# Kernel tuning notes

Measured on AMD Instinct MI355X. Metric: run time of the kernel, lower is better.

## Reference

```python
import jax, jax.numpy as jnp
import numpy as np

IMG = 840.0
MIN_SIZES = [[16.0, 32.0], [64.0, 128.0], [256.0, 512.0]]
STEPS = [8, 16, 32]
THRESH = 0.35      # neg_overlap / matching threshold used by this repo's MultiBoxLoss
NEG_POS = 7
LOC_WEIGHT = 2.0
VAR0, VAR1 = 0.1, 0.2


def _make_priors():
    out = []
    for ms, step in zip(MIN_SIZES, STEPS):
        f = int(np.ceil(IMG / step))
        jj, ii = np.meshgrid(np.arange(f), np.arange(f))  # j: cols (x), i: rows (y)
        cx = (jj + 0.5) * step / IMG
        cy = (ii + 0.5) * step / IMG
        for m in ms:
            s = np.full_like(cx, m / IMG)
            out.append(np.stack([cx, cy, s, s], axis=-1).reshape(-1, 4))
    return np.concatenate(out, axis=0).astype(np.float32)  # [29126, 4] (cx, cy, w, h)


def setup_inputs() -> dict:
    key = jax.random.key(0)
    k1, k2, k3, k4 = jax.random.split(key, 4)
    B, G = 64, 24
    priors = jnp.asarray(_make_priors())            # [P, 4]
    P = priors.shape[0]
    loc_data = 0.1 * jax.random.normal(k1, (B, P, 4), dtype=jnp.float32)
    conf_data = jax.random.normal(k2, (B, P, 2), dtype=jnp.float32)
    cxy = jax.random.uniform(k3, (B, G, 2), minval=0.2, maxval=0.8)
    wh = jax.random.uniform(k4, (B, G, 2), minval=0.05, maxval=0.3)
    gt_boxes = jnp.clip(jnp.concatenate([cxy - wh / 2, cxy + wh / 2], axis=-1), 1e-3, 1.0)
    gt_labels = jnp.ones((B, G), dtype=jnp.int32)   # single foreground class (num_classes=2)
    return {"loc_data": loc_data, "conf_data": conf_data, "gt_boxes": gt_boxes,
            "gt_labels": gt_labels, "priors": priors}


def _multibox_loss(loc_data, conf_data, gt_boxes, gt_labels, priors):
    B, P, _ = loc_data.shape
    G = gt_boxes.shape[1]
    # priors in point form for IoU
    pr_pt = jnp.concatenate([priors[:, :2] - priors[:, 2:] / 2,
                             priors[:, :2] + priors[:, 2:] / 2], axis=1)  # [P,4]
    area_p = (pr_pt[:, 2] - pr_pt[:, 0]) * (pr_pt[:, 3] - pr_pt[:, 1])

    def match_one(truths, labels):
        # IoU [G, P]
        lt = jnp.maximum(truths[:, None, :2], pr_pt[None, :, :2])
        rb = jnp.minimum(truths[:, None, 2:], pr_pt[None, :, 2:])
        wh = jnp.clip(rb - lt, 0.0)
        inter = wh[..., 0] * wh[..., 1]
        area_t = (truths[:, 2] - truths[:, 0]) * (truths[:, 3] - truths[:, 1])
        iou = inter / (area_t[:, None] + area_p[None, :] - inter)
        best_prior_idx = jnp.argmax(iou, axis=1)          # [G]
        bto = jnp.max(iou, axis=0)                        # [P] best truth overlap
        bti = jnp.argmax(iou, axis=0)                     # [P] best truth idx
        bto = bto.at[best_prior_idx].set(2.0)             # ensure each gt keeps its best prior
        bti = bti.at[best_prior_idx].set(jnp.arange(G))
        matched = truths[bti]                             # [P,4]
        conf = jnp.where(bto < THRESH, 0, labels[bti])    # [P]
        # encode (SSD style, variances 0.1/0.2)
        g_cxcy = ((matched[:, :2] + matched[:, 2:]) / 2 - priors[:, :2]) / (VAR0 * priors[:, 2:])
        g_wh = jnp.log((matched[:, 2:] - matched[:, :2]) / priors[:, 2:]) / VAR1
        return jnp.concatenate([g_cxcy, g_wh], axis=1), conf

    loc_t, conf_t = jax.vmap(match_one)(gt_boxes, gt_labels)  # [B,P,4], [B,P]
    pos = conf_t > 0                                          # [B,P]

    # localization: smooth L1 over positives
    diff = jnp.abs(loc_data - loc_t)
    sl1 = jnp.where(diff < 1.0, 0.5 * diff * diff, diff - 0.5)
    loss_l = jnp.sum(sl1 * pos[..., None].astype(loc_data.dtype))

    # per-prior CE = logsumexp - logit[target]
    lse = jax.nn.logsumexp(conf_data, axis=-1)                               # [B,P]
    gold = jnp.take_along_axis(conf_data, conf_t[..., None], axis=-1)[..., 0]
    ce_all = lse - gold                                                      # [B,P]

    # hard negative mining: rank background-class loss of negatives
    mine = jnp.where(pos, 0.0, ce_all)
    rank = jnp.argsort(jnp.argsort(-mine, axis=1), axis=1)
    num_pos = jnp.sum(pos, axis=1, keepdims=True)                            # [B,1]
    num_neg = jnp.minimum(NEG_POS * num_pos, P - 1)
    neg = rank < num_neg

    mask = pos | neg
    loss_c = jnp.sum(jnp.where(mask, ce_all, 0.0))

    N = jnp.maximum(jnp.sum(pos).astype(loc_data.dtype), 1.0)
    return loss_l / N, loss_c / N


def reference(loc_data, conf_data, gt_boxes, gt_labels, priors):
    loss_l, loss_c = _multibox_loss(loc_data, conf_data, gt_boxes, gt_labels, priors)
    return LOC_WEIGHT * loss_l + loss_c
```

## Files before the change

### kernel.cpp

```cpp
#include <hip/hip_runtime.h>

static constexpr int B_ = 64;
static constexpr int P_ = 29126;
static constexpr int G_ = 24;
static constexpr float THRESH_ = 0.35f;
static constexpr int NEGPOS_ = 7;
static constexpr int PBC_ = (P_ + 2047) / 2048;
static constexpr int NBLK_ = PBC_ * B_;
static constexpr int CCSTRIDE_ = 32;

static constexpr size_t ZBYTES_ =
    (size_t)B_*P_ + (size_t)B_*4096*4 + (size_t)B_*CCSTRIDE_*4;
static constexpr int ZVEC_ = (int)((ZBYTES_ + 15) / 16);

__global__ __launch_bounds__(256) void k_zero(ulonglong2* __restrict__ dst)
{
    const int i = blockIdx.x*256 + threadIdx.x;
    if (i < ZVEC_) dst[i] = make_ulonglong2(0ull, 0ull);
}

__global__ __launch_bounds__(256) void k_sparse(
    const float4* __restrict__ gt4,
    const float4* __restrict__ priors4,
    unsigned char* __restrict__ match,
    unsigned long long* __restrict__ bp_pack)
{
    const int g = blockIdx.x;
    const int b = blockIdx.y;
    const int bg = b*G_ + g;
    const int tid = threadIdx.x;

    const float4 t = gt4[bg];
    const float area_t = (t.z - t.x) * (t.w - t.y);

    float bv = -1.0f; int bq = 0;

#pragma unroll
    for (int r = 0; r < 6; ++r) {
        const int   f    = (r < 2) ? 105 : (r < 4) ? 53 : 27;
        const float sc   = (r < 2) ? 105.0f : (r < 4) ? 52.5f : 26.25f;
        const int   base = (r == 0) ? 0 : (r == 1) ? 11025 : (r == 2) ? 22050
                         : (r == 3) ? 24859 : (r == 4) ? 27668 : 28397;
        const float hw   = ((r == 0) ? 16.0f : (r == 1) ? 32.0f : (r == 2) ? 64.0f
                         : (r == 3) ? 128.0f : (r == 4) ? 256.0f : 512.0f)
                           * (0.5f / 840.0f);

        const int j0 = max(0,     (int)floorf((t.x - hw)*sc - 0.5f) - 1);
        const int j1 = min(f - 1, (int)ceilf ((t.z + hw)*sc - 0.5f) + 1);
        const int i0 = max(0,     (int)floorf((t.y - hw)*sc - 0.5f) - 1);
        const int i1 = min(f - 1, (int)ceilf ((t.w + hw)*sc - 0.5f) + 1);
        const int W = j1 - j0 + 1;
        const int n = W * (i1 - i0 + 1);

        for (int c = tid; c < n; c += 256) {
            const int ii = c / W;
            const int jj = c - ii*W;
            const int p = base + (i0 + ii)*f + (j0 + jj);
            const float4 pr = priors4[p];
            const float hx = pr.z * 0.5f, hy = pr.w * 0.5f;
            const float px0 = pr.x - hx, py0 = pr.y - hy;
            const float px1 = pr.x + hx, py1 = pr.y + hy;
            const float area_p = (px1 - px0) * (py1 - py0);
            const float lx = fmaxf(t.x, px0), ly = fmaxf(t.y, py0);
            const float rx = fminf(t.z, px1), ry = fminf(t.w, py1);
            const float iw = fmaxf(rx - lx, 0.0f), ih = fmaxf(ry - ly, 0.0f);
            const float inter = iw * ih;
            const float iou = __fdividef(inter, (area_t + area_p) - inter);

            if (iou >= THRESH_) match[(size_t)b*P_ + p] = 1;
            if (iou > bv) { bv = iou; bq = p; }
        }
    }

    const int lane = tid & 63, wave = tid >> 6;
    for (int m = 32; m; m >>= 1) {
        const float ov = __shfl_xor(bv, m, 64);
        const int   oq = __shfl_xor(bq, m, 64);
        if (ov > bv || (ov == bv && oq < bq)) { bv = ov; bq = oq; }
    }
    __shared__ float swv[4];
    __shared__ int   swq[4];
    if (lane == 0) { swv[wave] = bv; swq[wave] = bq; }
    __syncthreads();
    if (tid == 0) {
        float v = swv[0]; int q = swq[0];
#pragma unroll
        for (int w = 1; w < 4; ++w)
            if (swv[w] > v || (swv[w] == v && swq[w] < q)) { v = swv[w]; q = swq[w]; }
        bp_pack[bg] = (v >= 0.0f)
            ? (((unsigned long long)__float_as_uint(v) << 32)
               | (unsigned long long)(~(unsigned int)q))
            : 0ull;
    }
}

__global__ __launch_bounds__(256) void k_loss(
    const float4* __restrict__ loc4,
    const float2* __restrict__ conf2,
    const float4* __restrict__ gt4,
    const int* __restrict__ labels,
    const float4* __restrict__ priors4,
    const unsigned char* __restrict__ match,
    const unsigned long long* __restrict__ bp_pack,
    float* __restrict__ mine,
    float* __restrict__ pl, float* __restrict__ pc, int* __restrict__ pp,
    unsigned int* __restrict__ hist1)
{
    const int b = blockIdx.y;
    const int tid = threadIdx.x;
    __shared__ float4 sgt[G_];
    __shared__ float  sarea[G_];
    __shared__ int    sbpi[G_];
    __shared__ int    slab[G_];
    __shared__ unsigned int shist[4096];
    if (tid < G_) {
        const float4 t = gt4[b*G_ + tid];
        sgt[tid] = t;
        sarea[tid] = (t.z - t.x) * (t.w - t.y);
        sbpi[tid] = (int)(~(unsigned int)(bp_pack[b*G_ + tid] & 0xFFFFFFFFull));
        slab[tid] = labels[b*G_ + tid];
    }
    for (int i = tid; i < 4096; i += 256) shist[i] = 0;
    __syncthreads();

    float lL = 0.0f, pce = 0.0f; int np = 0;

#pragma unroll
    for (int c = 0; c < 8; ++c) {
        const int p = blockIdx.x*2048 + c*256 + tid;
        if (p < P_) {
            const int idx = b*P_ + p;
            const unsigned char fl = match[idx];

            int og = -1;
#pragma unroll
            for (int g = 0; g < G_; ++g)
                if (sbpi[g] == p) og = g;

            int cc = 0, g = 0;
            if (og >= 0) { g = og; cc = slab[g]; }
            else if (fl) {
                const float4 pr = priors4[p];
                const float hx = pr.z * 0.5f, hy = pr.w * 0.5f;
                const float px0 = pr.x - hx, py0 = pr.y - hy;
                const float px1 = pr.x + hx, py1 = pr.y + hy;
                const float area_p = (px1 - px0) * (py1 - py0);
                float best = -1.0f;
#pragma unroll
                for (int gg = 0; gg < G_; ++gg) {
                    const float4 t = sgt[gg];
                    const float lx = fmaxf(t.x, px0), ly = fmaxf(t.y, py0);
                    const float rx = fminf(t.z, px1), ry = fminf(t.w, py1);
                    const float iw = fmaxf(rx - lx, 0.0f), ih = fmaxf(ry - ly, 0.0f);
                    const float inter = iw * ih;
                    const float iou = __fdividef(inter, (sarea[gg] + area_p) - inter);
                    if (iou > best) { best = iou; g = gg; }
                }
                cc = slab[g];
            }

            const float2 x = conf2[idx];
            const float z = (cc == 0) ? (x.y - x.x) : (x.x - x.y);
            const float ce = __logf(1.0f + __expf(z));

            float mv = ce;
            if (cc > 0) {
                np += 1; pce += ce; mv = 0.0f;
                const float4 t  = sgt[g];
                const float4 pr = priors4[p];
                const float gcx = __fdividef((t.x + t.z)*0.5f - pr.x, 0.1f*pr.z);
                const float gcy = __fdividef((t.y + t.w)*0.5f - pr.y, 0.1f*pr.w);
                const float gw  = __logf(__fdividef(t.z - t.x, pr.z)) * 5.0f;
                const float gh  = __logf(__fdividef(t.w - t.y, pr.w)) * 5.0f;
                const float4 l = loc4[idx];
                const float d0 = fabsf(l.x - gcx);
                const float d1 = fabsf(l.y - gcy);
                const float d2 = fabsf(l.z - gw);
                const float d3 = fabsf(l.w - gh);
                lL += (d0 < 1.0f) ? 0.5f*d0*d0 : d0 - 0.5f;
                lL += (d1 < 1.0f) ? 0.5f*d1*d1 : d1 - 0.5f;
                lL += (d2 < 1.0f) ? 0.5f*d2*d2 : d2 - 0.5f;
                lL += (d3 < 1.0f) ? 0.5f*d3*d3 : d3 - 0.5f;
            }
            mine[idx] = mv;
            atomicAdd(&shist[__float_as_uint(mv) >> 20], 1u);
        }
    }

    __shared__ float sL[256], sC[256];
    __shared__ int   sP[256];
    sL[tid] = lL; sC[tid] = pce; sP[tid] = np;
    __syncthreads();
    for (int off = 128; off > 0; off >>= 1) {
        if (tid < off) {
            sL[tid] += sL[tid+off];
            sC[tid] += sC[tid+off];
            sP[tid] += sP[tid+off];
        }
        __syncthreads();
    }
    if (tid == 0) {
        const int o = b*PBC_ + blockIdx.x;
        pl[o] = sL[0]; pc[o] = sC[0]; pp[o] = sP[0];
    }
    for (int i = tid; i < 4096; i += 256) {
        const unsigned int h = shist[i];
        if (h) atomicAdd(&hist1[b*4096 + i], h);
    }
}

__global__ __launch_bounds__(256) void k_sel1(
    const unsigned int* __restrict__ hist1, const int* __restrict__ pp,
    int2* __restrict__ sel)
{
    const int b = blockIdx.x;
    const int tid = threadIdx.x;
    __shared__ int sred[256];
    sred[tid] = (tid < PBC_) ? pp[b*PBC_ + tid] : 0;
    __syncthreads();
    for (int off = 128; off > 0; off >>= 1) {
        if (tid < off) sred[tid] += sred[tid+off];
        __syncthreads();
    }
    const int np = sred[0];
    __syncthreads();
    int k = NEGPOS_ * np; if (k > P_-1) k = P_-1;
    if (k <= 0) { if (tid == 0) sel[b] = make_int2(0x7FFFFFFF, 0); return; }

    const unsigned int* h = hist1 + b*4096;
    const int rbase = 16*tid;
    int s = 0;
#pragma unroll
    for (int i = 0; i < 16; ++i) s += (int)h[4095 - (rbase + i)];
    __shared__ int S[256];
    S[tid] = s;
    __syncthreads();
    for (int off = 1; off < 256; off <<= 1) {
        const int t = (tid >= off) ? S[tid-off] : 0;
        __syncthreads();
        S[tid] += t;
        __syncthreads();
    }
    const int Sprev = tid ? S[tid-1] : 0;
    if (S[tid] >= k && Sprev < k) {
        int cum = Sprev;
        for (int i = 0; i < 16; ++i) {
            const int c = (int)h[4095 - (rbase + i)];
            cum += c;
            if (cum >= k) {
                sel[b] = make_int2(4095 - (rbase + i), k - (cum - c));
                break;
            }
        }
    }
}

__global__ __launch_bounds__(256) void k_collect(
    const float* __restrict__ mine, const int2* __restrict__ sel,
    unsigned int* __restrict__ cand, int* __restrict__ candCount,
    float* __restrict__ pcol)
{
    const int b = blockIdx.y;
    const int tid = threadIdx.x;
    const int t1 = sel[b].x;
    const int lane = tid & 63;

    __shared__ unsigned int sbuf[2048];
    __shared__ int scnt;
    __shared__ int gbase;
    if (tid == 0) scnt = 0;
    __syncthreads();

    float sum = 0.0f;
#pragma unroll
    for (int c = 0; c < 8; ++c) {
        const int p = blockIdx.x*2048 + c*256 + tid;
        bool isCand = false;
        unsigned int u = 0;
        if (p < P_) {
            const float v = mine[(size_t)b*P_ + p];
            u = __float_as_uint(v);
            const int bin = (int)(u >> 20);
            if (bin > t1) sum += v;
            else isCand = (bin == t1);
        }
        const unsigned long long mask = __ballot(isCand);
        const int wcnt = __popcll(mask);
        int wbase = 0;
        if (lane == 0 && wcnt) wbase = atomicAdd(&scnt, wcnt);
        wbase = __shfl(wbase, 0, 64);
        if (isCand) {
            const int before = __popcll(mask & ((1ull << lane) - 1ull));
            sbuf[wbase + before] = u;
        }
    }
    __syncthreads();
    const int tot = scnt;
    if (tid == 0) gbase = tot ? atomicAdd(&candCount[b*CCSTRIDE_], tot) : 0;
    __syncthreads();
    for (int i = tid; i < tot; i += 256)
        cand[(size_t)b*P_ + gbase + i] = sbuf[i];

    __shared__ float sf[256];
    sf[tid] = sum;
    __syncthreads();
    for (int off = 128; off > 0; off >>= 1) {
        if (tid < off) sf[tid] += sf[tid+off];
        __syncthreads();
    }
    if (tid == 0) pcol[b*PBC_ + blockIdx.x] = sf[0];
}

__global__ __launch_bounds__(256) void k_sel2(
    const unsigned int* __restrict__ cand, const int* __restrict__ candCount,
    const int2* __restrict__ sel, const float* __restrict__ pcol,
    float* __restrict__ ctop)
{
    const int b = blockIdx.x;
    const int tid = threadIdx.x;
    __shared__ float sf[256];
    sf[tid] = (tid < PBC_) ? pcol[b*PBC_ + tid] : 0.0f;
    __syncthreads();
    for (int off = 128; off > 0; off >>= 1) {
        if (tid < off) sf[tid] += sf[tid+off];
        __syncthreads();
    }
    const float sumhi = sf[0];
    __syncthreads();

    const int2 se = sel[b];
    const int t1 = se.x, kk = se.y;
    if (kk <= 0) { if (tid == 0) ctop[b] = 0.0f; return; }
    const int nc = candCount[b*CCSTRIDE_];
    const unsigned int* row = cand + (size_t)b * P_;

    __shared__ unsigned int hist[1024];
    __shared__ int S[256];
    __shared__ int sh_b1, sh_kk2, sh_b0;

    for (int i = tid; i < 1024; i += 256) hist[i] = 0;
    __syncthreads();
    for (int i = tid; i < nc; i += 256)
        atomicAdd(&hist[(row[i] >> 10) & 1023u], 1u);
    __syncthreads();
    {
        const int rbase = 4*tid;
        int ls = 0;
#pragma unroll
        for (int i = 0; i < 4; ++i) ls += (int)hist[1023 - (rbase + i)];
        S[tid] = ls;
        __syncthreads();
        for (int off = 1; off < 256; off <<= 1) {
            const int t = (tid >= off) ? S[tid-off] : 0;
            __syncthreads();
            S[tid] += t;
            __syncthreads();
        }
        const int Sprev = tid ? S[tid-1] : 0;
        if (S[tid] >= kk && Sprev < kk) {
            int cum = Sprev;
            for (int i = 0; i < 4; ++i) {
                const int c = (int)hist[1023 - (rbase + i)];
                cum += c;
                if (cum >= kk) {
                    sh_b1 = 1023 - (rbase + i);
                    sh_kk2 = kk - (cum - c);
                    break;
                }
            }
        }
    }
    __syncthreads();
    const int b1 = sh_b1, kk2 = sh_kk2;

    __syncthreads();
    for (int i = tid; i < 1024; i += 256) hist[i] = 0;
    __syncthreads();
    for (int i = tid; i < nc; i += 256) {
        const unsigned int u = row[i];
        if (((u >> 10) & 1023u) == (unsigned int)b1)
            atomicAdd(&hist[u & 1023u], 1u);
    }
    __syncthreads();
    {
        const int rbase = 4*tid;
        int ls = 0;
#pragma unroll
        for (int i = 0; i < 4; ++i) ls += (int)hist[1023 - (rbase + i)];
        S[tid] = ls;
        __syncthreads();
        for (int off = 1; off < 256; off <<= 1) {
            const int t = (tid >= off) ? S[tid-off] : 0;
            __syncthreads();
            S[tid] += t;
            __syncthreads();
        }
        const int Sprev = tid ? S[tid-1] : 0;
        if (S[tid] >= kk2 && Sprev < kk2) {
            int cum = Sprev;
            for (int i = 0; i < 4; ++i) {
                const int c = (int)hist[1023 - (rbase + i)];
                cum += c;
                if (cum >= kk2) { sh_b0 = 1023 - (rbase + i); break; }
            }
        }
    }
    __syncthreads();
    const unsigned int Tbits =
        ((unsigned int)t1 << 20) | ((unsigned int)b1 << 10) | (unsigned int)sh_b0;
    const float T = __uint_as_float(Tbits);

    float sumc = 0.0f; int cnt = 0;
    for (int i = tid; i < nc; i += 256) {
        const unsigned int u = row[i];
        if (u > Tbits) { sumc += __uint_as_float(u); ++cnt; }
    }
    __shared__ int sci[256];
    sf[tid] = sumc; sci[tid] = cnt;
    __syncthreads();
    for (int off = 128; off > 0; off >>= 1) {
        if (tid < off) { sf[tid] += sf[tid+off]; sci[tid] += sci[tid+off]; }
        __syncthreads();
    }
    if (tid == 0)
        ctop[b] = sumhi + sf[0] + (float)(kk - sci[0]) * T;
}

__global__ __launch_bounds__(256) void k_final(
    const float* __restrict__ pl, const float* __restrict__ pc,
    const int* __restrict__ pp, const float* __restrict__ ctop,
    float* __restrict__ out)
{
    const int tid = threadIdx.x;
    float sL = 0.0f, sC = 0.0f; int tp = 0;
    for (int i = tid; i < NBLK_; i += 256) {
        sL += pl[i]; sC += pc[i]; tp += pp[i];
    }
    float sT = (tid < B_) ? ctop[tid] : 0.0f;
    __shared__ float aL[256], aC[256], aT[256];
    __shared__ int   aP[256];
    aL[tid] = sL; aC[tid] = sC; aT[tid] = sT; aP[tid] = tp;
    __syncthreads();
    for (int off = 128; off > 0; off >>= 1) {
        if (tid < off) {
            aL[tid] += aL[tid+off];
            aC[tid] += aC[tid+off];
            aT[tid] += aT[tid+off];
            aP[tid] += aP[tid+off];
        }
        __syncthreads();
    }
    if (tid == 0) {
        const float N = fmaxf((float)aP[0], 1.0f);
        out[0] = (2.0f*aL[0] + aC[0] + aT[0]) / N;
    }
}

extern "C" void kernel_launch(void* const* d_in, const int* in_sizes, int n_in,
                              void* d_out, int out_size, void* d_ws, size_t ws_size,
                              hipStream_t stream)
{
    const float* loc    = (const float*)d_in[0];
    const float* conf   = (const float*)d_in[1];
    const float* gt     = (const float*)d_in[2];
    const int*   labels = (const int*)d_in[3];
    const float* priors = (const float*)d_in[4];
    float* out = (float*)d_out;

    char* ws = (char*)d_ws;
    size_t off = 0;
    unsigned char* match = (unsigned char*)(ws + off); off += (size_t)B_*P_;
    unsigned int* hist1 = (unsigned int*)(ws + off);   off += (size_t)B_*4096*4;
    int* candCount = (int*)(ws + off);                 off += (size_t)B_*CCSTRIDE_*4;
    off = (off + 255) & ~255ull;
    unsigned long long* bp_pack =
        (unsigned long long*)(ws + off);             off += (size_t)B_*G_*8;
    float* mine = (float*)(ws + off);                off += (size_t)B_*P_*4;
    float* pl   = (float*)(ws + off);                off += (size_t)NBLK_*4;
    float* pc   = (float*)(ws + off);                off += (size_t)NBLK_*4;
    int*   pp   = (int*)(ws + off);                  off += (size_t)NBLK_*4;
    float* pcol = (float*)(ws + off);                off += (size_t)NBLK_*4;
    unsigned int* cand = (unsigned int*)(ws + off);  off += (size_t)B_*P_*4;
    int2*  sel  = (int2*)(ws + off);                 off += (size_t)B_*8;
    float* ctop = (float*)(ws + off);                off += (size_t)B_*4;

    k_zero<<<dim3((ZVEC_ + 255)/256), dim3(256), 0, stream>>>((ulonglong2*)ws);
    k_sparse<<<dim3(G_, B_), dim3(256), 0, stream>>>(
        (const float4*)gt, (const float4*)priors, match, bp_pack);
    k_loss<<<dim3(PBC_, B_), dim3(256), 0, stream>>>(
        (const float4*)loc, (const float2*)conf, (const float4*)gt, labels,
        (const float4*)priors, match, bp_pack, mine, pl, pc, pp, hist1);
    k_sel1<<<dim3(B_), dim3(256), 0, stream>>>(hist1, pp, sel);
    k_collect<<<dim3(PBC_, B_), dim3(256), 0, stream>>>(mine, sel, cand, candCount, pcol);
    k_sel2<<<dim3(B_), dim3(256), 0, stream>>>(cand, candCount, sel, pcol, ctop);
    k_final<<<dim3(1), dim3(256), 0, stream>>>(pl, pc, pp, ctop, out);
}
```

Measured before the change: 76.90 us.

## Replace per-prior histogram with fixed threshold ladder counts and radix select

The shared-memory atomic histogram in the loss kernel is replaced by 16 fixed float thresholds. Each thread counts how many mined losses exceed each threshold in packed 16-bit register counters, which also removes the global histogram atomics and its zeroing. Blocks now cover 1024 priors instead of 2048, and the per-prior scan over 24 best-prior indices becomes a shared-memory override table. The exact selection is now a 4-pass 8-bit radix select over the candidates between two ladder thresholds. The tradeoff is that the coarser ladder can let many more candidates through, which adds work to the collect and select stages.

After: 75.69 us. Within noise of the previous version (-1.6%).

```diff
diff --git a/kernel.cpp b/kernel.cpp
--- a/kernel.cpp
+++ b/kernel.cpp
@@ -5,12 +5,15 @@
 static constexpr int G_ = 24;
 static constexpr float THRESH_ = 0.35f;
 static constexpr int NEGPOS_ = 7;
-static constexpr int PBC_ = (P_ + 2047) / 2048;
-static constexpr int NBLK_ = PBC_ * B_;
+static constexpr int PBL_ = (P_ + 1023) / 1024;
+static constexpr int NBL_ = PBL_ * B_;
 static constexpr int CCSTRIDE_ = 32;
 
-static constexpr size_t ZBYTES_ =
-    (size_t)B_*P_ + (size_t)B_*4096*4 + (size_t)B_*CCSTRIDE_*4;
+__device__ const float LAD_[16] = {
+    0.5f,    0.5901f, 0.6964f, 0.8220f, 0.9701f, 1.1450f, 1.3514f, 1.5950f,
+    1.8825f, 2.2218f, 2.6223f, 3.0950f, 3.6529f, 4.3113f, 5.0885f, 6.0057f };
+
+static constexpr size_t ZBYTES_ = (size_t)B_*P_ + (size_t)B_*CCSTRIDE_*4;
 static constexpr int ZVEC_ = (int)((ZBYTES_ + 15) / 16);
 
 __global__ __launch_bounds__(256) void k_zero(ulonglong2* __restrict__ dst)
@@ -104,42 +107,46 @@
     const unsigned long long* __restrict__ bp_pack,
     float* __restrict__ mine,
     float* __restrict__ pl, float* __restrict__ pc, int* __restrict__ pp,
-    unsigned int* __restrict__ hist1)
+    unsigned int* __restrict__ pcnt)
 {
     const int b = blockIdx.y;
     const int tid = threadIdx.x;
+    const int pbase = blockIdx.x*1024;
+
     __shared__ float4 sgt[G_];
     __shared__ float  sarea[G_];
-    __shared__ int    sbpi[G_];
     __shared__ int    slab[G_];
-    __shared__ unsigned int shist[4096];
+    __shared__ signed char sovr[1024];
     if (tid < G_) {
         const float4 t = gt4[b*G_ + tid];
         sgt[tid] = t;
         sarea[tid] = (t.z - t.x) * (t.w - t.y);
-        sbpi[tid] = (int)(~(unsigned int)(bp_pack[b*G_ + tid] & 0xFFFFFFFFull));
         slab[tid] = labels[b*G_ + tid];
     }
-    for (int i = tid; i < 4096; i += 256) shist[i] = 0;
+    for (int i = tid; i < 1024; i += 256) sovr[i] = -1;
+    __syncthreads();
+    if (tid == 0) {
+        for (int g = 0; g < G_; ++g) {
+            const int q = (int)(~(unsigned int)(bp_pack[b*G_ + g] & 0xFFFFFFFFull))
+                        - pbase;
+            if (q >= 0 && q < 1024) sovr[q] = (signed char)g;
+        }
+    }
     __syncthreads();
 
     float lL = 0.0f, pce = 0.0f; int np = 0;
-
-#pragma unroll
-    for (int c = 0; c < 8; ++c) {
-        const int p = blockIdx.x*2048 + c*256 + tid;
+    unsigned q0 = 0, q1 = 0, q2 = 0, q3 = 0, q4 = 0, q5 = 0, q6 = 0, q7 = 0;
+
+#pragma unroll
+    for (int c = 0; c < 4; ++c) {
+        const int p = pbase + c*256 + tid;
         if (p < P_) {
             const int idx = b*P_ + p;
-            const unsigned char fl = match[idx];
-
-            int og = -1;
-#pragma unroll
-            for (int g = 0; g < G_; ++g)
-                if (sbpi[g] == p) og = g;
+            const int og = (int)sovr[c*256 + tid];
 
             int cc = 0, g = 0;
             if (og >= 0) { g = og; cc = slab[g]; }
-            else if (fl) {
+            else if (match[idx]) {
                 const float4 pr = priors4[p];
                 const float hx = pr.z * 0.5f, hy = pr.w * 0.5f;
                 const float px0 = pr.x - hx, py0 = pr.y - hy;
@@ -183,89 +190,111 @@
                 lL += (d3 < 1.0f) ? 0.5f*d3*d3 : d3 - 0.5f;
             }
             mine[idx] = mv;
-            atomicAdd(&shist[__float_as_uint(mv) >> 20], 1u);
+
+            q0 += (unsigned)(mv > 0.5f)    + ((unsigned)(mv > 0.5901f) << 16);
+            q1 += (unsigned)(mv > 0.6964f) + ((unsigned)(mv > 0.8220f) << 16);
+            q2 += (unsigned)(mv > 0.9701f) + ((unsigned)(mv > 1.1450f) << 16);
+            q3 += (unsigned)(mv > 1.3514f) + ((unsigned)(mv > 1.5950f) << 16);
+            q4 += (unsigned)(mv > 1.8825f) + ((unsigned)(mv > 2.2218f) << 16);
+            q5 += (unsigned)(mv > 2.6223f) + ((unsigned)(mv > 3.0950f) << 16);
+            q6 += (unsigned)(mv > 3.6529f) + ((unsigned)(mv > 4.3113f) << 16);
+            q7 += (unsigned)(mv > 5.0885f) + ((unsigned)(mv > 6.0057f) << 16);
         }
     }
 
     __shared__ float sL[256], sC[256];
     __shared__ int   sP[256];
+    __shared__ unsigned su[8][256];
     sL[tid] = lL; sC[tid] = pce; sP[tid] = np;
+    su[0][tid] = q0; su[1][tid] = q1; su[2][tid] = q2; su[3][tid] = q3;
+    su[4][tid] = q4; su[5][tid] = q5; su[6][tid] = q6; su[7][tid] = q7;
     __syncthreads();
     for (int off = 128; off > 0; off >>= 1) {
         if (tid < off) {
             sL[tid] += sL[tid+off];
             sC[tid] += sC[tid+off];
             sP[tid] += sP[tid+off];
-        }
-        __syncthreads();
-    }
+#pragma unroll
+            for (int j = 0; j < 8; ++j) su[j][tid] += su[j][tid+off];
+        }
+        __syncthreads();
+    }
+    const int o = b*PBL_ + blockIdx.x;
+    if (tid == 0) { pl[o] = sL[0]; pc[o] = sC[0]; pp[o] = sP[0]; }
+    if (tid < 8) pcnt[o*8 + tid] = su[tid][0];
+}
+
+__global__ __launch_bounds__(256) void k_sel1(
+    const unsigned int* __restrict__ pcnt, const int* __restrict__ pp,
+    int4* __restrict__ sel)
+{
+    const int b = blockIdx.x;
+    const int tid = threadIdx.x;
+    __shared__ int sred[256];
+    sred[tid] = (tid < PBL_) ? pp[b*PBL_ + tid] : 0;
+    __syncthreads();
+    for (int off = 128; off > 0; off >>= 1) {
+        if (tid < off) sred[tid] += sred[tid+off];
+        __syncthreads();
+    }
+    const int np = sred[0];
+    int k = NEGPOS_ * np; if (k > P_-1) k = P_-1;
+
+    __shared__ unsigned red[32][8];
+    {
+        const int i = tid >> 3, j = tid & 7;
+        red[i][j] = (i < PBL_) ? pcnt[(b*PBL_ + i)*8 + j] : 0u;
+    }
+    __syncthreads();
+    for (int off = 16; off > 0; off >>= 1) {
+        const int i = tid >> 3, j = tid & 7;
+        if (i < off) red[i][j] += red[i+off][j];
+        __syncthreads();
+    }
+    __shared__ int C[16];
+    if (tid < 8) {
+        C[2*tid]   = (int)(red[0][tid] & 0xFFFFu);
+        C[2*tid+1] = (int)(red[0][tid] >> 16);
+    }
+    __syncthreads();
     if (tid == 0) {
-        const int o = b*PBC_ + blockIdx.x;
-        pl[o] = sL[0]; pc[o] = sC[0]; pp[o] = sP[0];
-    }
-    for (int i = tid; i < 4096; i += 256) {
-        const unsigned int h = shist[i];
-        if (h) atomicAdd(&hist1[b*4096 + i], h);
-    }
-}
-
-__global__ __launch_bounds__(256) void k_sel1(
-    const unsigned int* __restrict__ hist1, const int* __restrict__ pp,
-    int2* __restrict__ sel)
-{
-    const int b = blockIdx.x;
-    const int tid = threadIdx.x;
-    __shared__ int sred[256];
-    sred[tid] = (tid < PBC_) ? pp[b*PBC_ + tid] : 0;
-    __syncthreads();
-    for (int off = 128; off > 0; off >>= 1) {
-        if (tid < off) sred[tid] += sred[tid+off];
-        __syncthreads();
-    }
-    const int np = sred[0];
-    __syncthreads();
-    int k = NEGPOS_ * np; if (k > P_-1) k = P_-1;
-    if (k <= 0) { if (tid == 0) sel[b] = make_int2(0x7FFFFFFF, 0); return; }
-
-    const unsigned int* h = hist1 + b*4096;
-    const int rbase = 16*tid;
-    int s = 0;
-#pragma unroll
-    for (int i = 0; i < 16; ++i) s += (int)h[4095 - (rbase + i)];
-    __shared__ int S[256];
-    S[tid] = s;
-    __syncthreads();
-    for (int off = 1; off < 256; off <<= 1) {
-        const int t = (tid >= off) ? S[tid-off] : 0;
-        __syncthreads();
-        S[tid] += t;
-        __syncthreads();
-    }
-    const int Sprev = tid ? S[tid-1] : 0;
-    if (S[tid] >= k && Sprev < k) {
-        int cum = Sprev;
-        for (int i = 0; i < 16; ++i) {
-            const int c = (int)h[4095 - (rbase + i)];
-            cum += c;
-            if (cum >= k) {
-                sel[b] = make_int2(4095 - (rbase + i), k - (cum - c));
-                break;
+        int4 s; s.w = 0;
+        if (k <= 0) {
+            s.x = 0x7F800000; s.y = 0x7F800000; s.z = 0;
+        } else {
+            int js = -1;
+            for (int j = 0; j < 16; ++j) if (C[j] >= k) js = j;
+            if (js < 0) {
+                s.x = __float_as_int(LAD_[0]);
+                s.y = __float_as_int(-1.0f);
+                s.z = k - C[0];
+            } else if (js == 15) {
+                s.x = 0x7F800000;
+                s.y = __float_as_int(LAD_[15]);
+                s.z = k;
+            } else {
+                s.x = __float_as_int(LAD_[js+1]);
+                s.y = __float_as_int(LAD_[js]);
+                s.z = k - C[js+1];
             }
         }
+        sel[b] = s;
     }
 }
 
 __global__ __launch_bounds__(256) void k_collect(
-    const float* __restrict__ mine, const int2* __restrict__ sel,
+    const float* __restrict__ mine, const int4* __restrict__ sel,
     unsigned int* __restrict__ cand, int* __restrict__ candCount,
     float* __restrict__ pcol)
 {
     const int b = blockIdx.y;
     const int tid = threadIdx.x;
-    const int t1 = sel[b].x;
     const int lane = tid & 63;
-
-    __shared__ unsigned int sbuf[2048];
+    const int4 se = sel[b];
+    const float hi = __int_as_float(se.x);
+    const float lo = __int_as_float(se.y);
+
+    __shared__ unsigned int sbuf[1024];
     __shared__ int scnt;
     __shared__ int gbase;
     if (tid == 0) scnt = 0;
@@ -273,16 +302,15 @@
 
     float sum = 0.0f;
 #pragma unroll
-    for (int c = 0; c < 8; ++c) {
-        const int p = blockIdx.x*2048 + c*256 + tid;
+    for (int c = 0; c < 4; ++c) {
+        const int p = blockIdx.x*1024 + c*256 + tid;
         bool isCand = false;
         unsigned int u = 0;
         if (p < P_) {
             const float v = mine[(size_t)b*P_ + p];
             u = __float_as_uint(v);
-            const int bin = (int)(u >> 20);
-            if (bin > t1) sum += v;
-            else isCand = (bin == t1);
+            if (v > hi) sum += v;
+            else isCand = (v > lo);
         }
         const unsigned long long mask = __ballot(isCand);
         const int wcnt = __popcll(mask);
@@ -308,18 +336,18 @@
         if (tid < off) sf[tid] += sf[tid+off];
         __syncthreads();
     }
-    if (tid == 0) pcol[b*PBC_ + blockIdx.x] = sf[0];
+    if (tid == 0) pcol[b*PBL_ + blockIdx.x] = sf[0];
 }
 
 __global__ __launch_bounds__(256) void k_sel2(
     const unsigned int* __restrict__ cand, const int* __restrict__ candCount,
-    const int2* __restrict__ sel, const float* __restrict__ pcol,
+    const int4* __restrict__ sel, const float* __restrict__ pcol,
     float* __restrict__ ctop)
 {
     const int b = blockIdx.x;
     const int tid = threadIdx.x;
     __shared__ float sf[256];
-    sf[tid] = (tid < PBC_) ? pcol[b*PBC_ + tid] : 0.0f;
+    sf[tid] = (tid < PBL_) ? pcol[b*PBL_ + tid] : 0.0f;
     __syncthreads();
     for (int off = 128; off > 0; off >>= 1) {
         if (tid < off) sf[tid] += sf[tid+off];
@@ -328,95 +356,60 @@
     const float sumhi = sf[0];
     __syncthreads();
 
-    const int2 se = sel[b];
-    const int t1 = se.x, kk = se.y;
-    if (kk <= 0) { if (tid == 0) ctop[b] = 0.0f; return; }
+    const int kk = sel[b].z;
     const int nc = candCount[b*CCSTRIDE_];
+    if (kk <= 0 || nc <= 0) { if (tid == 0) ctop[b] = sumhi; return; }
     const unsigned int* row = cand + (size_t)b * P_;
 
-    __shared__ unsigned int hist[1024];
-    __shared__ int S[256];
-    __shared__ int sh_b1, sh_kk2, sh_b0;
-
-    for (int i = tid; i < 1024; i += 256) hist[i] = 0;
-    __syncthreads();
-    for (int i = tid; i < nc; i += 256)
-        atomicAdd(&hist[(row[i] >> 10) & 1023u], 1u);
-    __syncthreads();
-    {
-        const int rbase = 4*tid;
-        int ls = 0;
-#pragma unroll
-        for (int i = 0; i < 4; ++i) ls += (int)hist[1023 - (rbase + i)];
-        S[tid] = ls;
-        __syncthreads();
+    __shared__ unsigned int hist[256];
+    __shared__ unsigned int sc0[256], sc1[256];
+    __shared__ unsigned int sh_prefix;
+    __shared__ int sh_kk;
+
+    unsigned int prefix = 0; int kk2 = kk;
+    for (int pass = 3; pass >= 0; --pass) {
+        hist[tid] = 0;
+        __syncthreads();
+        const unsigned int highmask =
+            (pass == 3) ? 0u : (0xFFFFFFFFu << ((pass+1)*8));
+        for (int i = tid; i < nc; i += 256) {
+            const unsigned int u = row[i];
+            if ((u & highmask) == (prefix & highmask))
+                atomicAdd(&hist[(u >> (pass*8)) & 255u], 1u);
+        }
+        __syncthreads();
+        sc0[tid] = hist[255 - tid];
+        __syncthreads();
+        unsigned int* src = sc0; unsigned int* dst = sc1;
         for (int off = 1; off < 256; off <<= 1) {
-            const int t = (tid >= off) ? S[tid-off] : 0;
+            unsigned int v = src[tid];
+            if (tid >= off) v += src[tid - off];
+            dst[tid] = v;
             __syncthreads();
-            S[tid] += t;
-            __syncthreads();
-        }
-        const int Sprev = tid ? S[tid-1] : 0;
-        if (S[tid] >= kk && Sprev < kk) {
-            int cum = Sprev;
-            for (int i = 0; i < 4; ++i) {
-                const int c = (int)hist[1023 - (rbase + i)];
-                cum += c;
-                if (cum >= kk) {
-                    sh_b1 = 1023 - (rbase + i);
-                    sh_kk2 = kk - (cum - c);
-                    break;
-                }
+            unsigned int* t = src; src = dst; dst = t;
+        }
+        {
+            const int bin = 255 - tid;
+            const int cum = (int)src[tid];
+            const int cumPrev = (tid == 0) ? 0 : (int)src[tid-1];
+            if (cum >= kk2 && cumPrev < kk2) {
+                sh_prefix = prefix | ((unsigned int)bin << (pass*8));
+                sh_kk = kk2 - cumPrev;
             }
         }
-    }
-    __syncthreads();
-    const int b1 = sh_b1, kk2 = sh_kk2;
-
-    __syncthreads();
-    for (int i = tid; i < 1024; i += 256) hist[i] = 0;
-    __syncthreads();
+        __syncthreads();
+        prefix = sh_prefix; kk2 = sh_kk;
+        __syncthreads();
+    }
+
+    const float T = __uint_as_float(prefix);
+    float sum = 0.0f; int cnt = 0;
     for (int i = tid; i < nc; i += 256) {
         const unsigned int u = row[i];
-        if (((u >> 10) & 1023u) == (unsigned int)b1)
-            atomicAdd(&hist[u & 1023u], 1u);
-    }
-    __syncthreads();
-    {
-        const int rbase = 4*tid;
-        int ls = 0;
-#pragma unroll
-        for (int i = 0; i < 4; ++i) ls += (int)hist[1023 - (rbase + i)];
-        S[tid] = ls;
-        __syncthreads();
-        for (int off = 1; off < 256; off <<= 1) {
-            const int t = (tid >= off) ? S[tid-off] : 0;
-            __syncthreads();
-            S[tid] += t;
-            __syncthreads();
-        }
-        const int Sprev = tid ? S[tid-1] : 0;
-        if (S[tid] >= kk2 && Sprev < kk2) {
-            int cum = Sprev;
-            for (int i = 0; i < 4; ++i) {
-                const int c = (int)hist[1023 - (rbase + i)];
-                cum += c;
-                if (cum >= kk2) { sh_b0 = 1023 - (rbase + i); break; }
-            }
-        }
-    }
-    __syncthreads();
-    const unsigned int Tbits =
-        ((unsigned int)t1 << 20) | ((unsigned int)b1 << 10) | (unsigned int)sh_b0;
-    const float T = __uint_as_float(Tbits);
-
-    float sumc = 0.0f; int cnt = 0;
-    for (int i = tid; i < nc; i += 256) {
-        const unsigned int u = row[i];
-        if (u > Tbits) { sumc += __uint_as_float(u); ++cnt; }
+        if (u > prefix) { sum += __uint_as_float(u); ++cnt; }
     }
     __shared__ int sci[256];
-    sf[tid] = sumc; sci[tid] = cnt;
+    sf[tid] = sum; sci[tid] = cnt;
     __syncthreads();
     for (int off = 128; off > 0; off >>= 1) {
         if (tid < off) { sf[tid] += sf[tid+off]; sci[tid] += sci[tid+off]; }
@@ -433,7 +426,7 @@
 {
     const int tid = threadIdx.x;
     float sL = 0.0f, sC = 0.0f; int tp = 0;
-    for (int i = tid; i < NBLK_; i += 256) {
+    for (int i = tid; i < NBL_; i += 256) {
         sL += pl[i]; sC += pc[i]; tp += pp[i];
     }
     float sT = (tid < B_) ? ctop[tid] : 0.0f;
@@ -470,28 +463,28 @@
     char* ws = (char*)d_ws;
     size_t off = 0;
     unsigned char* match = (unsigned char*)(ws + off); off += (size_t)B_*P_;
-    unsigned int* hist1 = (unsigned int*)(ws + off);   off += (size_t)B_*4096*4;
     int* candCount = (int*)(ws + off);                 off += (size_t)B_*CCSTRIDE_*4;
     off = (off + 255) & ~255ull;
     unsigned long long* bp_pack =
         (unsigned long long*)(ws + off);             off += (size_t)B_*G_*8;
     float* mine = (float*)(ws + off);                off += (size_t)B_*P_*4;
-    float* pl   = (float*)(ws + off);                off += (size_t)NBLK_*4;
-    float* pc   = (float*)(ws + off);                off += (size_t)NBLK_*4;
-    int*   pp   = (int*)(ws + off);                  off += (size_t)NBLK_*4;
-    float* pcol = (float*)(ws + off);                off += (size_t)NBLK_*4;
+    float* pl   = (float*)(ws + off);                off += (size_t)NBL_*4;
+    float* pc   = (float*)(ws + off);                off += (size_t)NBL_*4;
+    int*   pp   = (int*)(ws + off);                  off += (size_t)NBL_*4;
+    float* pcol = (float*)(ws + off);                off += (size_t)NBL_*4;
+    unsigned int* pcnt = (unsigned int*)(ws + off);  off += (size_t)NBL_*8*4;
     unsigned int* cand = (unsigned int*)(ws + off);  off += (size_t)B_*P_*4;
-    int2*  sel  = (int2*)(ws + off);                 off += (size_t)B_*8;
+    int4*  sel  = (int4*)(ws + off);                 off += (size_t)B_*16;
     float* ctop = (float*)(ws + off);                off += (size_t)B_*4;
 
     k_zero<<<dim3((ZVEC_ + 255)/256), dim3(256), 0, stream>>>((ulonglong2*)ws);
     k_sparse<<<dim3(G_, B_), dim3(256), 0, stream>>>(
         (const float4*)gt, (const float4*)priors, match, bp_pack);
-    k_loss<<<dim3(PBC_, B_), dim3(256), 0, stream>>>(
+    k_loss<<<dim3(PBL_, B_), dim3(256), 0, stream>>>(
         (const float4*)loc, (const float2*)conf, (const float4*)gt, labels,
-        (const float4*)priors, match, bp_pack, mine, pl, pc, pp, hist1);
-    k_sel1<<<dim3(B_), dim3(256), 0, stream>>>(hist1, pp, sel);
-    k_collect<<<dim3(PBC_, B_), dim3(256), 0, stream>>>(mine, sel, cand, candCount, pcol);
+        (const float4*)priors, match, bp_pack, mine, pl, pc, pp, pcnt);
+    k_sel1<<<dim3(B_), dim3(256), 0, stream>>>(pcnt, pp, sel);
+    k_collect<<<dim3(PBL_, B_), dim3(256), 0, stream>>>(mine, sel, cand, candCount, pcol);
     k_sel2<<<dim3(B_), dim3(256), 0, stream>>>(cand, candCount, sel, pcol, ctop);
     k_final<<<dim3(1), dim3(256), 0, stream>>>(pl, pc, pp, ctop, out);
 }
```
